# Optimization experiments

Hardware: AMD Instinct MI355X
Metric: run time of the kernel (lower is better)

The kernel has to match this reference:

```python
import jax, jax.numpy as jnp
import numpy as np

B, T, E, H = 2, 2048, 768, 12
DH = E // H  # per-head attention dim
EPS = 1e-5


def setup_inputs() -> dict:
    key = jax.random.key(0)
    ks = jax.random.split(key, 12)
    s = 0.02
    return {
        "x": jax.random.normal(ks[0], (B, T, E), dtype=jnp.float32),
        # stacked per-head projection weights: [H, E, DH], biases [H, DH]
        "Wq": jax.random.normal(ks[1], (H, E, DH), dtype=jnp.float32) * s,
        "bq": jax.random.normal(ks[2], (H, DH), dtype=jnp.float32) * s,
        "Wk": jax.random.normal(ks[3], (H, E, DH), dtype=jnp.float32) * s,
        "bk": jax.random.normal(ks[4], (H, DH), dtype=jnp.float32) * s,
        "Wv": jax.random.normal(ks[5], (H, E, DH), dtype=jnp.float32) * s,
        "bv": jax.random.normal(ks[6], (H, DH), dtype=jnp.float32) * s,
        "Wo": jax.random.normal(ks[7], (E, E), dtype=jnp.float32) * s,
        "bo": jax.random.normal(ks[8], (E,), dtype=jnp.float32) * s,
        "gamma": jnp.ones((E,), dtype=jnp.float32),
        "beta": jnp.zeros((E,), dtype=jnp.float32),
    }


def reference(x, Wq, bq, Wk, bk, Wv, bv, Wo, bo, gamma, beta):
    # per-head projections (heads stacked on axis h)
    q = jnp.einsum("bte,hed->bhtd", x, Wq) + bq[None, :, None, :]
    k = jnp.einsum("bte,hed->bhtd", x, Wk) + bk[None, :, None, :]
    v = jnp.einsum("bte,hed->bhtd", x, Wv) + bv[None, :, None, :]

    scores = jnp.einsum("bhtd,bhsd->bhts", q, k) / jnp.sqrt(jnp.float32(DH))
    causal = jnp.tril(jnp.ones((T, T), dtype=bool))  # True = keep
    scores = jnp.where(causal[None, None], scores, -jnp.inf)
    attn = jax.nn.softmax(scores, axis=-1)
    o = jnp.einsum("bhts,bhsd->bhtd", attn, v)  # [B,H,T,DH]

    # concat heads in head order -> [B,T,E]
    concat = jnp.transpose(o, (0, 2, 1, 3)).reshape(B, T, E)
    proj = concat @ Wo + bo

    # LayerNorm(proj) then residual add
    mu = jnp.mean(proj, axis=-1, keepdims=True)
    var = jnp.mean((proj - mu) ** 2, axis=-1, keepdims=True)
    normed = (proj - mu) * jax.lax.rsqrt(var + EPS) * gamma + beta
    return x + normed
```

## Files before the change

kernel.cpp:

```cpp
#include <hip/hip_runtime.h>
#include <stdint.h>

#define NROWS 4096
#define EMB   768
#define NQKV  2304
#define TSEQ  2048
#define VTSTR 2080
#define XSTR  800
#define WSTR  800
#define PSTR  800
#define NHEAD 12
#define NBH   24

typedef unsigned short u16;
typedef u16  ushort4v __attribute__((ext_vector_type(4)));
typedef u16  ushort8 __attribute__((ext_vector_type(8)));
typedef __bf16 bf16x8 __attribute__((ext_vector_type(8)));
typedef float f32x4 __attribute__((ext_vector_type(4)));

typedef const __attribute__((address_space(1))) void* gas_ptr;
typedef __attribute__((address_space(3))) void* las_ptr;

__device__ __forceinline__ u16 f2bf(float f) {
  union { float f; uint32_t u; } v; v.f = f;
  uint32_t u = v.u;
  return (u16)((u + 0x7fffu + ((u >> 16) & 1u)) >> 16);
}
__device__ __forceinline__ float bf2f(u16 u) {
  union { uint32_t u; float f; } v; v.u = ((uint32_t)u) << 16;
  return v.f;
}
__device__ __forceinline__ uint32_t cvtpk(float lo, float hi) {
  uint32_t r;
  asm("v_cvt_pk_bf16_f32 %0, %1, %2" : "=v"(r) : "v"(lo), "v"(hi));
  return r;
}

#define VMCNT0 asm volatile("s_waitcnt vmcnt(0)" ::: "memory")
#define LGKM0  asm volatile("s_waitcnt lgkmcnt(0)" ::: "memory")
#define SBAR   __builtin_amdgcn_s_barrier()
#define SCHED0 __builtin_amdgcn_sched_barrier(0)
#define MFMA(a, b, c) __builtin_amdgcn_mfma_f32_16x16x32_bf16((a), (b), (c), 0, 0, 0)

__global__ __launch_bounds__(256) void k_pack(const float* __restrict__ x, u16* __restrict__ xb,
                                              const float* __restrict__ Wq, const float* __restrict__ Wk,
                                              const float* __restrict__ Wv, u16* __restrict__ wt,
                                              const float* __restrict__ Wo, u16* __restrict__ wot,
                                              uint32_t* __restrict__ cnt, uint32_t* __restrict__ tbl) {
  int bid = blockIdx.x, tid = threadIdx.x;
  if (bid == 0) {
    if (tid < 8) cnt[tid] = 0;
    if (tid >= 64 && tid < 144) {
      int p = tid - 64;
      int myqb = 0, myc = 0, k = 0;
      for (int qb = 0; qb < 32; ++qb) {
        int nch = (qb + 8) >> 3;
        for (int c = 0; c < nch; ++c) { if (k == p) { myqb = qb; myc = c; } ++k; }
      }
      int t0 = myc * 8;
      int t1 = (myqb + 1 < t0 + 8) ? myqb + 1 : t0 + 8;
      int mylen = t1 - t0, myid = myqb * 4 + myc;
      int rank = 0;
      for (int qb = 0; qb < 32; ++qb) {
        int nch = (qb + 8) >> 3;
        for (int c = 0; c < nch; ++c) {
          int u0 = c * 8;
          int u1 = (qb + 1 < u0 + 8) ? qb + 1 : u0 + 8;
          int l = u1 - u0, id = qb * 4 + c;
          if (l > mylen || (l == mylen && id < myid)) ++rank;
        }
      }
      tbl[rank] = (uint32_t)myqb | ((uint32_t)t0 << 8) | ((uint32_t)t1 << 16)
                | ((uint32_t)myc << 24) | (myqb <= 7 ? 0x80000000u : 0u);
    }
  }
  if (bid < 1536) {
    int i = bid * 2048 + tid * 8;
    int row = i / EMB, col = i - row * EMB;
    float4 a = *(const float4*)(x + i);
    float4 b = *(const float4*)(x + i + 4);
    uint4 o;
    o.x = cvtpk(a.x, a.y); o.y = cvtpk(a.z, a.w);
    o.z = cvtpk(b.x, b.y); o.w = cvtpk(b.z, b.w);
    *(uint4*)(xb + (size_t)row * XSTR + col) = o;
    return;
  }
  __shared__ u16 lds[64][68];
  if (bid < 1968) {
    int t = bid - 1536;
    int sel = t / 144, rest = t - sel * 144;
    int h = rest / 12, ec = rest - h * 12;
    const float* W = sel == 0 ? Wq : (sel == 1 ? Wk : Wv);
    const float* src = W + ((size_t)(h * EMB + ec * 64) * 64);
    int e = tid >> 2, d0 = (tid & 3) * 16;
#pragma unroll
    for (int j = 0; j < 4; ++j) {
      float4 v = *(const float4*)(src + (size_t)e * 64 + d0 + 4 * j);
      ushort4v pk;
      uint32_t w0 = cvtpk(v.x, v.y), w1 = cvtpk(v.z, v.w);
      pk[0] = (u16)(w0 & 0xffff); pk[1] = (u16)(w0 >> 16);
      pk[2] = (u16)(w1 & 0xffff); pk[3] = (u16)(w1 >> 16);
      *(ushort4v*)(&lds[e][d0 + 4 * j]) = pk;
    }
    __syncthreads();
    int d = tid >> 2, e0 = (tid & 3) * 16;
    ushort8 o0, o1;
#pragma unroll
    for (int j = 0; j < 8; ++j) { o0[j] = lds[e0 + j][d]; o1[j] = lds[e0 + 8 + j][d]; }
    int n = sel * EMB + h * 64 + d;
    u16* dst = wt + (size_t)n * WSTR + ec * 64 + e0;
    *(ushort8*)dst = o0;
    *(ushort8*)(dst + 8) = o1;
  } else {
    int t = bid - 1968;
    int er = t / 12, nc = t - er * 12;
    int e = tid >> 2, n0 = (tid & 3) * 16;
#pragma unroll
    for (int j = 0; j < 4; ++j) {
      float4 v = *(const float4*)(Wo + (size_t)(er * 64 + e) * EMB + nc * 64 + n0 + 4 * j);
      ushort4v pk;
      uint32_t w0 = cvtpk(v.x, v.y), w1 = cvtpk(v.z, v.w);
      pk[0] = (u16)(w0 & 0xffff); pk[1] = (u16)(w0 >> 16);
      pk[2] = (u16)(w1 & 0xffff); pk[3] = (u16)(w1 >> 16);
      *(ushort4v*)(&lds[e][n0 + 4 * j]) = pk;
    }
    __syncthreads();
    int n = tid >> 2, e0 = (tid & 3) * 16;
    ushort8 o0, o1;
#pragma unroll
    for (int j = 0; j < 8; ++j) { o0[j] = lds[e0 + j][n]; o1[j] = lds[e0 + 8 + j][n]; }
    u16* dst = wot + (size_t)(nc * 64 + n) * WSTR + er * 64 + e0;
    *(ushort8*)dst = o0;
    *(ushort8*)(dst + 8) = o1;
  }
}

template<int BM, int BN, int OUT_MODE>
__global__ __launch_bounds__(256) void k_gemm(const u16* __restrict__ A, const u16* __restrict__ Bt,
                                              const float* __restrict__ b0, const float* __restrict__ b1,
                                              const float* __restrict__ b2, void* __restrict__ Cout,
                                              u16* __restrict__ qpk, u16* __restrict__ kpk,
                                              u16* __restrict__ vtout,
                                              int M, int N, int K, int lda, int ldb) {
  constexpr int MR = BM / 32, NR = BN / 32;
  __shared__ u16 lds_a[BM * 64];
  __shared__ u16 lds_b[BN * 64];
  int tid = threadIdx.x;
  int w = tid >> 6, lane = tid & 63;
  int wr = w >> 1, wc = w & 1;
  int m0 = blockIdx.x * BM, n0 = blockIdx.y * BN;
  int lrow = lane & 15, g = lane >> 4;

  f32x4 zero = {0.f, 0.f, 0.f, 0.f};
  f32x4 acc[MR][NR];
  for (int m = 0; m < MR; ++m) for (int n = 0; n < NR; ++n) acc[m][n] = zero;

  int l8 = lane >> 3, c8 = lane & 7;

  for (int k0 = 0; k0 < K; k0 += 64) {
#pragma unroll
    for (int i = 0; i < BM / 32; ++i) {
      int row = w * (BM / 4) + 8 * i + l8;
      int c16 = c8 ^ (row & 7);
      const u16* ga = A + (size_t)(m0 + row) * lda + k0 + c16 * 8;
      __builtin_amdgcn_global_load_lds((gas_ptr)ga, (las_ptr)(lds_a + (w * (BM / 4) + 8 * i) * 64), 16, 0, 0);
    }
#pragma unroll
    for (int i = 0; i < BN / 32; ++i) {
      int row = w * (BN / 4) + 8 * i + l8;
      int c16 = c8 ^ (row & 7);
      const u16* gb = Bt + (size_t)(n0 + row) * ldb + k0 + c16 * 8;
      __builtin_amdgcn_global_load_lds((gas_ptr)gb, (las_ptr)(lds_b + (w * (BN / 4) + 8 * i) * 64), 16, 0, 0);
    }
    __syncthreads();
    bf16x8 af[MR][2], bfr[NR][2];
#pragma unroll
    for (int m = 0; m < MR; ++m)
#pragma unroll
      for (int kc = 0; kc < 2; ++kc) {
        int row = wr * (BM / 2) + m * 16 + lrow;
        int ch = (kc * 4 + g) ^ (row & 7);
        af[m][kc] = *(const bf16x8*)(lds_a + row * 64 + ch * 8);
      }
#pragma unroll
    for (int n = 0; n < NR; ++n)
#pragma unroll
      for (int kc = 0; kc < 2; ++kc) {
        int row = wc * (BN / 2) + n * 16 + lrow;
        int ch = (kc * 4 + g) ^ (row & 7);
        bfr[n][kc] = *(const bf16x8*)(lds_b + row * 64 + ch * 8);
      }
#pragma unroll
    for (int kc = 0; kc < 2; ++kc)
#pragma unroll
      for (int m = 0; m < MR; ++m)
#pragma unroll
        for (int n = 0; n < NR; ++n)
          acc[m][n] = MFMA(af[m][kc], bfr[n][kc], acc[m][n]);
    __syncthreads();
  }

#pragma unroll
  for (int m = 0; m < MR; ++m)
#pragma unroll
    for (int n = 0; n < NR; ++n) {
      int col = n0 + wc * (BN / 2) + n * 16 + lrow;
      float bcol;
      if (OUT_MODE == 1) bcol = b0[col];
      else {
        int sel = col >= 1536 ? 2 : (col >= 768 ? 1 : 0);
        const float* bs = sel == 0 ? b0 : (sel == 1 ? b1 : b2);
        bcol = bs[col - sel * EMB];
      }
      int row0 = m0 + wr * (BM / 2) + m * 16 + 4 * g;
      if (OUT_MODE == 2) {
        int sel = col >= 1536 ? 2 : (col >= 768 ? 1 : 0);
        int c = col - sel * EMB;
        int hh = c >> 6, d = c & 63;
        int bb = row0 >> 11, t = row0 & 2047;
        int y = bb * NHEAD + hh;
        if (sel == 2) {
          ushort4v pk;
#pragma unroll
          for (int r = 0; r < 4; ++r) pk[r] = f2bf(acc[m][n][r] + bcol);
          *(ushort4v*)(vtout + (size_t)(y * 64 + d) * VTSTR + t) = pk;
        } else {
          u16* dst = (sel == 0 ? qpk : kpk) + (size_t)(y * TSEQ + t) * 64 + d;
#pragma unroll
          for (int r = 0; r < 4; ++r) dst[r * 64] = f2bf(acc[m][n][r] + bcol);
        }
      } else {
#pragma unroll
        for (int r = 0; r < 4; ++r) {
          int row = row0 + r;
          ((float*)Cout)[(size_t)row * PSTR + col] = acc[m][n][r] + bcol;
        }
      }
    }
}

__global__ __launch_bounds__(256, 4) void k_attn(const u16* __restrict__ qpk, const u16* __restrict__ kpk,
                                                 const u16* __restrict__ vt,
                                                 u16* __restrict__ aout, uint32_t* __restrict__ cnt,
                                                 const uint32_t* __restrict__ tbl,
                                                 u16* __restrict__ pO, float* __restrict__ pL) {
  __shared__ u16 kbuf[2][64 * 64];
  __shared__ u16 vbuf[2][64 * 64];
  __shared__ u16 pbuf[4][16 * 64];
  int tid = threadIdx.x;
  int w = tid >> 6, lane = tid & 63;
  int ql = lane & 15, g = lane >> 4;
  int xcd = blockIdx.x & 7;
  const float sc2 = 0.18033688f;
  u16* pw = &pbuf[w][0];
  int swz = (ql & 7) << 3;
  int l8 = lane >> 3, c8 = lane & 7;
  volatile int* taskp = (volatile int*)&pbuf[0][0];
  f32x4 zero = {0.f, 0.f, 0.f, 0.f};

  for (;;) {
    if (tid == 0) *taskp = (int)atomicAdd(&cnt[xcd], 1u);
    __syncthreads();
    int tau = *taskp;
    __syncthreads();
    if (tau >= 240) break;

    int rank = tau / 3, yl = tau - rank * 3;
    uint32_t te = tbl[rank];
    int qb = te & 0xff, t0 = (te >> 8) & 0xff, t1ex = (te >> 16) & 0xff, cslot = (te >> 24) & 0x7f;
    bool direct = (te >> 31) != 0;

    int y = xcd * 3 + yl;
    int b = y / NHEAD, h = y - b * NHEAD;
    int qrow0w = qb * 64 + w * 16;
    int qg = qrow0w + ql;

    const u16* qp = qpk + (size_t)(y * TSEQ + qg) * 64;
    bf16x8 bq0 = *(const bf16x8*)(qp + g * 8);
    bf16x8 bq1 = *(const bf16x8*)(qp + 32 + g * 8);

    const u16* kst = kpk + (size_t)y * TSEQ * 64;
    const u16* vst = vt + (size_t)y * 64 * VTSTR;

    f32x4 o0 = zero, o1 = zero, o2 = zero, o3 = zero;
    float lr = 0.f;

    auto STAGE = [&](int bi, int t_) {
#pragma unroll
      for (int i = 0; i < 2; ++i) {
        int row = i * 32 + 8 * w + l8;
        int c16 = c8 ^ (row & 7);
        const u16* gk = kst + (size_t)t_ * 4096 + row * 64 + c16 * 8;
        __builtin_amdgcn_global_load_lds((gas_ptr)gk, (las_ptr)(&kbuf[bi][(i * 32 + 8 * w) * 64]), 16, 0, 0);
        const u16* gv = vst + (size_t)row * VTSTR + t_ * 64 + c16 * 8;
        __builtin_amdgcn_global_load_lds((gas_ptr)gv, (las_ptr)(&vbuf[bi][(i * 32 + 8 * w) * 64]), 16, 0, 0);
      }
    };

    STAGE(t0 & 1, t0);
    for (int t = t0; t < t1ex; ++t) {
      int cur = t & 1;
      VMCNT0;
      SBAR;
      if (t + 1 < t1ex) STAGE(cur ^ 1, t + 1);

      const u16* kb = &kbuf[cur][0];
      const u16* vb = &vbuf[cur][0];
      int s0 = t * 64;

      f32x4 st[4];
#pragma unroll
      for (int sblk = 0; sblk < 4; ++sblk) {
        int row = sblk * 16 + ql;
        bf16x8 ka0 = *(const bf16x8*)(kb + ((row * 64 + 8 * g) ^ swz));
        bf16x8 ka1 = *(const bf16x8*)(kb + ((row * 64 + 32 + 8 * g) ^ swz));
        f32x4 acc = zero;
        acc = MFMA(ka0, bq0, acc);
        acc = MFMA(ka1, bq1, acc);
        st[sblk] = acc;
      }

      bool lastt = (t == qb);
      float e[4][4];
#pragma unroll
      for (int sblk = 0; sblk < 4; ++sblk)
#pragma unroll
        for (int r = 0; r < 4; ++r) {
          float vv = __builtin_fmaf(st[sblk][r], sc2, -2.0f);
          if (lastt) {
            int sg = s0 + sblk * 16 + 4 * g + r;
            if (sg > qg) vv = -1e30f;
          }
          float ee = __builtin_amdgcn_exp2f(vv);
          e[sblk][r] = ee;
          lr += ee;
        }

#pragma unroll
      for (int sblk = 0; sblk < 4; ++sblk) {
        uint2 dw;
        dw.x = cvtpk(e[sblk][0], e[sblk][1]);
        dw.y = cvtpk(e[sblk][2], e[sblk][3]);
        *(uint2*)(pw + ((ql * 64 + sblk * 16 + 4 * g) ^ swz)) = dw;
      }
      LGKM0; SCHED0;
      bf16x8 ap0 = *(const bf16x8*)(pw + ((ql * 64 + 8 * g) ^ swz));
      bf16x8 ap1 = *(const bf16x8*)(pw + ((ql * 64 + 32 + 8 * g) ^ swz));

#pragma unroll
      for (int n = 0; n < 4; ++n) {
        int row = n * 16 + ql;
        bf16x8 vb0 = *(const bf16x8*)(vb + ((row * 64 + 8 * g) ^ swz));
        bf16x8 vb1 = *(const bf16x8*)(vb + ((row * 64 + 32 + 8 * g) ^ swz));
        f32x4* op = (n == 0) ? &o0 : (n == 1) ? &o1 : (n == 2) ? &o2 : &o3;
        *op = MFMA(ap0, vb0, *op);
        *op = MFMA(ap1, vb1, *op);
      }
    }

    float lw = lr;
    lw += __shfl_xor(lw, 16);
    lw += __shfl_xor(lw, 32);

    if (direct) {
      float linv = 1.0f / lw;
      float l0 = __shfl(linv, 4 * g + 0);
      float l1 = __shfl(linv, 4 * g + 1);
      float l2 = __shfl(linv, 4 * g + 2);
      float l3 = __shfl(linv, 4 * g + 3);
      u16* ab = aout + (size_t)(b * TSEQ + qrow0w + 4 * g) * XSTR + h * 64 + ql;
      ab[0 * XSTR + 0]  = f2bf(o0[0] * l0); ab[1 * XSTR + 0]  = f2bf(o0[1] * l1);
      ab[2 * XSTR + 0]  = f2bf(o0[2] * l2); ab[3 * XSTR + 0]  = f2bf(o0[3] * l3);
      ab[0 * XSTR + 16] = f2bf(o1[0] * l0); ab[1 * XSTR + 16] = f2bf(o1[1] * l1);
      ab[2 * XSTR + 16] = f2bf(o1[2] * l2); ab[3 * XSTR + 16] = f2bf(o1[3] * l3);
      ab[0 * XSTR + 32] = f2bf(o2[0] * l0); ab[1 * XSTR + 32] = f2bf(o2[1] * l1);
      ab[2 * XSTR + 32] = f2bf(o2[2] * l2); ab[3 * XSTR + 32] = f2bf(o2[3] * l3);
      ab[0 * XSTR + 48] = f2bf(o3[0] * l0); ab[1 * XSTR + 48] = f2bf(o3[1] * l1);
      ab[2 * XSTR + 48] = f2bf(o3[2] * l2); ab[3 * XSTR + 48] = f2bf(o3[3] * l3);
    } else {
      int blk2 = (y * 24 + (qb - 8)) * 4 + cslot;
      u16* po = pO + (size_t)blk2 * 4096;
      float* pl = pL + (size_t)blk2 * 64;
      if (g == 0) pl[w * 16 + ql] = lw;
      u16* pb2 = po + (w * 16 + 4 * g) * 64 + ql;
      pb2[0 * 64 + 0]  = f2bf(o0[0]); pb2[1 * 64 + 0]  = f2bf(o0[1]);
      pb2[2 * 64 + 0]  = f2bf(o0[2]); pb2[3 * 64 + 0]  = f2bf(o0[3]);
      pb2[0 * 64 + 16] = f2bf(o1[0]); pb2[1 * 64 + 16] = f2bf(o1[1]);
      pb2[2 * 64 + 16] = f2bf(o1[2]); pb2[3 * 64 + 16] = f2bf(o1[3]);
      pb2[0 * 64 + 32] = f2bf(o2[0]); pb2[1 * 64 + 32] = f2bf(o2[1]);
      pb2[2 * 64 + 32] = f2bf(o2[2]); pb2[3 * 64 + 32] = f2bf(o2[3]);
      pb2[0 * 64 + 48] = f2bf(o3[0]); pb2[1 * 64 + 48] = f2bf(o3[1]);
      pb2[2 * 64 + 48] = f2bf(o3[2]); pb2[3 * 64 + 48] = f2bf(o3[3]);
    }
  }
}

__global__ __launch_bounds__(256) void k_combine(const u16* __restrict__ pO, const float* __restrict__ pL,
                                                 u16* __restrict__ aout) {
  int blk = blockIdx.x;
  int y = blk / 24, q8 = blk - y * 24, qb = q8 + 8;
  int nch = (qb + 8) >> 3;
  int b = y / NHEAD, h = y - b * NHEAD;
  int tid = threadIdx.x;
  int row = tid >> 2, c0 = (tid & 3) * 16;
  float l = 0.f;
  for (int c = 0; c < nch; ++c) l += pL[((size_t)blk * 4 + c) * 64 + row];
  float rinv = 1.0f / l;
  float acc[16];
#pragma unroll
  for (int j = 0; j < 16; ++j) acc[j] = 0.f;
  for (int c = 0; c < nch; ++c) {
    const u16* p = pO + ((size_t)blk * 4 + c) * 4096 + row * 64 + c0;
    ushort8 a0 = *(const ushort8*)p;
    ushort8 a1 = *(const ushort8*)(p + 8);
#pragma unroll
    for (int j = 0; j < 8; ++j) { acc[j] += bf2f(a0[j]); acc[8 + j] += bf2f(a1[j]); }
  }
  ushort8 o0, o1;
#pragma unroll
  for (int j = 0; j < 8; j += 2) {
    uint32_t w0 = cvtpk(acc[j] * rinv, acc[j + 1] * rinv);
    o0[j] = (u16)(w0 & 0xffff); o0[j + 1] = (u16)(w0 >> 16);
    uint32_t w1 = cvtpk(acc[8 + j] * rinv, acc[9 + j] * rinv);
    o1[j] = (u16)(w1 & 0xffff); o1[j + 1] = (u16)(w1 >> 16);
  }
  u16* dst = aout + (size_t)(b * TSEQ + qb * 64 + row) * XSTR + h * 64 + c0;
  *(ushort8*)dst = o0;
  *(ushort8*)(dst + 8) = o1;
}

__global__ __launch_bounds__(256) void k_ln_res(const float* __restrict__ proj, const float* __restrict__ x,
                                                const float* __restrict__ gamma, const float* __restrict__ beta,
                                                float* __restrict__ out) {
  __shared__ float smem[2][4];
  int row = blockIdx.x;
  const float* pr = proj + (size_t)row * PSTR;
  const float* xr = x + (size_t)row * EMB;
  float* orow = out + (size_t)row * EMB;
  int tid = threadIdx.x;
  float v[3];
  float s = 0.f, s2 = 0.f;
#pragma unroll
  for (int i = 0; i < 3; ++i) { v[i] = pr[tid + 256 * i]; s += v[i]; s2 += v[i] * v[i]; }
#pragma unroll
  for (int m = 1; m < 64; m <<= 1) { s += __shfl_xor(s, m); s2 += __shfl_xor(s2, m); }
  int w = tid >> 6, lane = tid & 63;
  if (lane == 0) { smem[0][w] = s; smem[1][w] = s2; }
  __syncthreads();
  s  = smem[0][0] + smem[0][1] + smem[0][2] + smem[0][3];
  s2 = smem[1][0] + smem[1][1] + smem[1][2] + smem[1][3];
  float mu = s * (1.f / EMB);
  float var = s2 * (1.f / EMB) - mu * mu;
  float rstd = rsqrtf(var + 1e-5f);
#pragma unroll
  for (int i = 0; i < 3; ++i) {
    int c = tid + 256 * i;
    orow[c] = xr[c] + (v[i] - mu) * rstd * gamma[c] + beta[c];
  }
}

extern "C" void kernel_launch(void* const* d_in, const int* in_sizes, int n_in,
                              void* d_out, int out_size, void* d_ws, size_t ws_size,
                              hipStream_t stream) {
  const float* x     = (const float*)d_in[0];
  const float* Wq    = (const float*)d_in[1];
  const float* bq    = (const float*)d_in[2];
  const float* Wk    = (const float*)d_in[3];
  const float* bk    = (const float*)d_in[4];
  const float* Wv    = (const float*)d_in[5];
  const float* bv    = (const float*)d_in[6];
  const float* Wo    = (const float*)d_in[7];
  const float* bo    = (const float*)d_in[8];
  const float* gamma = (const float*)d_in[9];
  const float* beta  = (const float*)d_in[10];
  float* out = (float*)d_out;

  char* ws = (char*)d_ws;
  size_t off = 0;
  u16* xb    = (u16*)(ws + off); off += (size_t)NROWS * XSTR * 2;
  u16* wqkvt = (u16*)(ws + off); off += (size_t)NQKV * WSTR * 2;
  u16* wot   = (u16*)(ws + off); off += (size_t)EMB * WSTR * 2;
  uint32_t* cnt = (uint32_t*)(ws + off); off += 64;
  uint32_t* tbl = (uint32_t*)(ws + off); off += 512;
  u16* qpk   = (u16*)(ws + off); off += (size_t)NBH * TSEQ * 64 * 2;
  u16* kpk   = (u16*)(ws + off); off += (size_t)NBH * TSEQ * 64 * 2;
  u16* vt    = (u16*)(ws + off); off += (size_t)NBH * 64 * VTSTR * 2;
  u16* aout  = (u16*)(ws + off); off += (size_t)NROWS * XSTR * 2;
  u16* pO    = (u16*)(ws + off); off += (size_t)NBH * 24 * 4 * 4096 * 2;
  float* pL  = (float*)(ws + off); off += (size_t)NBH * 24 * 4 * 64 * 4;
  float* proj = (float*)qpk;

  k_pack<<<dim3(2112), 256, 0, stream>>>(x, xb, Wq, Wk, Wv, wqkvt, Wo, wot, cnt, tbl);
  k_gemm<128, 128, 2><<<dim3(NROWS / 128, NQKV / 128), 256, 0, stream>>>(
      xb, wqkvt, bq, bk, bv, nullptr, qpk, kpk, vt, NROWS, NQKV, EMB, XSTR, WSTR);
  k_attn<<<dim3(1024), 256, 0, stream>>>(qpk, kpk, vt, aout, cnt, tbl, pO, pL);
  k_combine<<<dim3(NBH * 24), 256, 0, stream>>>(pO, pL, aout);
  k_gemm<128, 64, 1><<<dim3(NROWS / 128, EMB / 64), 256, 0, stream>>>(
      aout, wot, bo, nullptr, nullptr, proj, nullptr, nullptr, nullptr, NROWS, EMB, EMB, XSTR, WSTR);
  k_ln_res<<<NROWS, 256, 0, stream>>>(proj, x, gamma, beta, out);
}
```

Measured before the change: 130.2 us.

## Enlarge attention query tile to 256 rows with 8 waves, 32 rows each

The attention kernel now processes 256 query rows per task, using 512-thread blocks where each wave handles two 16-row query groups. Each staged K/V tile is therefore reused by four times as many query rows, which cuts global and LDS loads per unit of work. The task table, the split/combine scheme and the workspace layout are rebuilt for the coarser tiles. In exchange there is more wasted masked work on diagonal tiles, fewer and larger tasks (60 per XCD) that may balance worse, and higher register pressure at two blocks per CU.

After: 118.1 us. 1.1x faster.

```diff
diff --git a/kernel.cpp b/kernel.cpp
--- a/kernel.cpp
+++ b/kernel.cpp
@@ -50,28 +50,31 @@
   int bid = blockIdx.x, tid = threadIdx.x;
   if (bid == 0) {
     if (tid < 8) cnt[tid] = 0;
-    if (tid >= 64 && tid < 144) {
+    if (tid >= 64 && tid < 84) {
       int p = tid - 64;
-      int myqb = 0, myc = 0, k = 0;
-      for (int qb = 0; qb < 32; ++qb) {
-        int nch = (qb + 8) >> 3;
-        for (int c = 0; c < nch; ++c) { if (k == p) { myqb = qb; myc = c; } ++k; }
+      int myqi = 0, myc = 0, k = 0;
+      for (int qi = 0; qi < 8; ++qi) {
+        int nt = 4 * qi + 4;
+        int nch = (nt + 7) >> 3;
+        for (int c = 0; c < nch; ++c) { if (k == p) { myqi = qi; myc = c; } ++k; }
       }
+      int nt = 4 * myqi + 4;
       int t0 = myc * 8;
-      int t1 = (myqb + 1 < t0 + 8) ? myqb + 1 : t0 + 8;
-      int mylen = t1 - t0, myid = myqb * 4 + myc;
+      int t1 = (nt < t0 + 8) ? nt : t0 + 8;
+      int mylen = t1 - t0, myid = myqi * 4 + myc;
       int rank = 0;
-      for (int qb = 0; qb < 32; ++qb) {
-        int nch = (qb + 8) >> 3;
+      for (int qi = 0; qi < 8; ++qi) {
+        int nt2 = 4 * qi + 4;
+        int nch = (nt2 + 7) >> 3;
         for (int c = 0; c < nch; ++c) {
           int u0 = c * 8;
-          int u1 = (qb + 1 < u0 + 8) ? qb + 1 : u0 + 8;
-          int l = u1 - u0, id = qb * 4 + c;
+          int u1 = (nt2 < u0 + 8) ? nt2 : u0 + 8;
+          int l = u1 - u0, id = qi * 4 + c;
           if (l > mylen || (l == mylen && id < myid)) ++rank;
         }
       }
-      tbl[rank] = (uint32_t)myqb | ((uint32_t)t0 << 8) | ((uint32_t)t1 << 16)
-                | ((uint32_t)myc << 24) | (myqb <= 7 ? 0x80000000u : 0u);
+      tbl[rank] = (uint32_t)myqi | ((uint32_t)t0 << 8) | ((uint32_t)t1 << 16)
+                | ((uint32_t)myc << 24) | (myqi <= 1 ? 0x80000000u : 0u);
     }
   }
   if (bid < 1536) {
@@ -239,14 +242,55 @@
     }
 }
 
-__global__ __launch_bounds__(256, 4) void k_attn(const u16* __restrict__ qpk, const u16* __restrict__ kpk,
+#define QKROW(SB) do { \
+    bf16x8 ka0 = *(const bf16x8*)(kb + ((((SB) * 16 + ql) * 64 + 8 * g) ^ swz)); \
+    bf16x8 ka1 = *(const bf16x8*)(kb + ((((SB) * 16 + ql) * 64 + 32 + 8 * g) ^ swz)); \
+    st##SB##q0 = MFMA(ka0, bq00, st##SB##q0); st##SB##q0 = MFMA(ka1, bq01, st##SB##q0); \
+    st##SB##q1 = MFMA(ka0, bq10, st##SB##q1); st##SB##q1 = MFMA(ka1, bq11, st##SB##q1); \
+  } while (0)
+
+#define SMX1(STV, SB, QC, LR) do { \
+    float _v0 = __builtin_fmaf(STV[0], sc2, -2.0f); \
+    float _v1 = __builtin_fmaf(STV[1], sc2, -2.0f); \
+    float _v2 = __builtin_fmaf(STV[2], sc2, -2.0f); \
+    float _v3 = __builtin_fmaf(STV[3], sc2, -2.0f); \
+    if (maskt) { \
+      int _sg = s0 + (SB) * 16 + 4 * g; \
+      int _qq = qw0 + (QC) * 16 + ql; \
+      if (_sg + 0 > _qq) _v0 = -1e30f; \
+      if (_sg + 1 > _qq) _v1 = -1e30f; \
+      if (_sg + 2 > _qq) _v2 = -1e30f; \
+      if (_sg + 3 > _qq) _v3 = -1e30f; \
+    } \
+    float _e0 = __builtin_amdgcn_exp2f(_v0), _e1 = __builtin_amdgcn_exp2f(_v1); \
+    float _e2 = __builtin_amdgcn_exp2f(_v2), _e3 = __builtin_amdgcn_exp2f(_v3); \
+    LR += (_e0 + _e1) + (_e2 + _e3); \
+    uint2 _dw; _dw.x = cvtpk(_e0, _e1); _dw.y = cvtpk(_e2, _e3); \
+    *(uint2*)(pw + ((((QC) * 16 + ql) * 64 + (SB) * 16 + 4 * g) ^ swz)) = _dw; \
+  } while (0)
+
+#define PVROW(DB) do { \
+    bf16x8 vb0 = *(const bf16x8*)(vb + ((((DB) * 16 + ql) * 64 + 8 * g) ^ swz)); \
+    bf16x8 vb1 = *(const bf16x8*)(vb + ((((DB) * 16 + ql) * 64 + 32 + 8 * g) ^ swz)); \
+    o##DB##q0 = MFMA(ap00, vb0, o##DB##q0); o##DB##q0 = MFMA(ap01, vb1, o##DB##q0); \
+    o##DB##q1 = MFMA(ap10, vb0, o##DB##q1); o##DB##q1 = MFMA(ap11, vb1, o##DB##q1); \
+  } while (0)
+
+#define OUTD(DB, QC, PTR, STRIDE, L0, L1, L2, L3) do { \
+    (PTR)[0 * (STRIDE) + (DB) * 16] = f2bf(o##DB##q##QC[0] * (L0)); \
+    (PTR)[1 * (STRIDE) + (DB) * 16] = f2bf(o##DB##q##QC[1] * (L1)); \
+    (PTR)[2 * (STRIDE) + (DB) * 16] = f2bf(o##DB##q##QC[2] * (L2)); \
+    (PTR)[3 * (STRIDE) + (DB) * 16] = f2bf(o##DB##q##QC[3] * (L3)); \
+  } while (0)
+
+__global__ __launch_bounds__(512, 2) void k_attn(const u16* __restrict__ qpk, const u16* __restrict__ kpk,
                                                  const u16* __restrict__ vt,
                                                  u16* __restrict__ aout, uint32_t* __restrict__ cnt,
                                                  const uint32_t* __restrict__ tbl,
                                                  u16* __restrict__ pO, float* __restrict__ pL) {
   __shared__ u16 kbuf[2][64 * 64];
   __shared__ u16 vbuf[2][64 * 64];
-  __shared__ u16 pbuf[4][16 * 64];
+  __shared__ u16 pbuf[8][32 * 64];
   int tid = threadIdx.x;
   int w = tid >> 6, lane = tid & 63;
   int ql = lane & 15, g = lane >> 4;
@@ -254,7 +298,7 @@
   const float sc2 = 0.18033688f;
   u16* pw = &pbuf[w][0];
   int swz = (ql & 7) << 3;
-  int l8 = lane >> 3, c8 = lane & 7;
+  int srow = tid >> 3, sc8 = tid & 7;
   volatile int* taskp = (volatile int*)&pbuf[0][0];
   f32x4 zero = {0.f, 0.f, 0.f, 0.f};
 
@@ -263,38 +307,38 @@
     __syncthreads();
     int tau = *taskp;
     __syncthreads();
-    if (tau >= 240) break;
+    if (tau >= 60) break;
 
     int rank = tau / 3, yl = tau - rank * 3;
     uint32_t te = tbl[rank];
-    int qb = te & 0xff, t0 = (te >> 8) & 0xff, t1ex = (te >> 16) & 0xff, cslot = (te >> 24) & 0x7f;
+    int qi = te & 0xff, t0 = (te >> 8) & 0xff, t1ex = (te >> 16) & 0xff, cslot = (te >> 24) & 0x7f;
     bool direct = (te >> 31) != 0;
 
     int y = xcd * 3 + yl;
     int b = y / NHEAD, h = y - b * NHEAD;
-    int qrow0w = qb * 64 + w * 16;
-    int qg = qrow0w + ql;
-
-    const u16* qp = qpk + (size_t)(y * TSEQ + qg) * 64;
-    bf16x8 bq0 = *(const bf16x8*)(qp + g * 8);
-    bf16x8 bq1 = *(const bf16x8*)(qp + 32 + g * 8);
+    int qb0 = qi * 256, qw0 = qb0 + w * 32;
+    int qtw = qw0 >> 6;
+
+    const u16* qp0 = qpk + (size_t)(y * TSEQ + qw0 + ql) * 64;
+    const u16* qp1 = qpk + (size_t)(y * TSEQ + qw0 + 16 + ql) * 64;
+    bf16x8 bq00 = *(const bf16x8*)(qp0 + 8 * g);
+    bf16x8 bq01 = *(const bf16x8*)(qp0 + 32 + 8 * g);
+    bf16x8 bq10 = *(const bf16x8*)(qp1 + 8 * g);
+    bf16x8 bq11 = *(const bf16x8*)(qp1 + 32 + 8 * g);
 
     const u16* kst = kpk + (size_t)y * TSEQ * 64;
     const u16* vst = vt + (size_t)y * 64 * VTSTR;
 
-    f32x4 o0 = zero, o1 = zero, o2 = zero, o3 = zero;
-    float lr = 0.f;
+    f32x4 o0q0 = zero, o1q0 = zero, o2q0 = zero, o3q0 = zero;
+    f32x4 o0q1 = zero, o1q1 = zero, o2q1 = zero, o3q1 = zero;
+    float lr0 = 0.f, lr1 = 0.f;
 
     auto STAGE = [&](int bi, int t_) {
-#pragma unroll
-      for (int i = 0; i < 2; ++i) {
-        int row = i * 32 + 8 * w + l8;
-        int c16 = c8 ^ (row & 7);
-        const u16* gk = kst + (size_t)t_ * 4096 + row * 64 + c16 * 8;
-        __builtin_amdgcn_global_load_lds((gas_ptr)gk, (las_ptr)(&kbuf[bi][(i * 32 + 8 * w) * 64]), 16, 0, 0);
-        const u16* gv = vst + (size_t)row * VTSTR + t_ * 64 + c16 * 8;
-        __builtin_amdgcn_global_load_lds((gas_ptr)gv, (las_ptr)(&vbuf[bi][(i * 32 + 8 * w) * 64]), 16, 0, 0);
-      }
+      int c16 = sc8 ^ (srow & 7);
+      const u16* gk = kst + (size_t)t_ * 4096 + srow * 64 + c16 * 8;
+      __builtin_amdgcn_global_load_lds((gas_ptr)gk, (las_ptr)(&kbuf[bi][(8 * w) * 64]), 16, 0, 0);
+      const u16* gv = vst + (size_t)srow * VTSTR + t_ * 64 + c16 * 8;
+      __builtin_amdgcn_global_load_lds((gas_ptr)gv, (las_ptr)(&vbuf[bi][(8 * w) * 64]), 16, 0, 0);
     };
 
     STAGE(t0 & 1, t0);
@@ -307,90 +351,51 @@
       const u16* kb = &kbuf[cur][0];
       const u16* vb = &vbuf[cur][0];
       int s0 = t * 64;
-
-      f32x4 st[4];
-#pragma unroll
-      for (int sblk = 0; sblk < 4; ++sblk) {
-        int row = sblk * 16 + ql;
-        bf16x8 ka0 = *(const bf16x8*)(kb + ((row * 64 + 8 * g) ^ swz));
-        bf16x8 ka1 = *(const bf16x8*)(kb + ((row * 64 + 32 + 8 * g) ^ swz));
-        f32x4 acc = zero;
-        acc = MFMA(ka0, bq0, acc);
-        acc = MFMA(ka1, bq1, acc);
-        st[sblk] = acc;
-      }
-
-      bool lastt = (t == qb);
-      float e[4][4];
-#pragma unroll
-      for (int sblk = 0; sblk < 4; ++sblk)
-#pragma unroll
-        for (int r = 0; r < 4; ++r) {
-          float vv = __builtin_fmaf(st[sblk][r], sc2, -2.0f);
-          if (lastt) {
-            int sg = s0 + sblk * 16 + 4 * g + r;
-            if (sg > qg) vv = -1e30f;
-          }
-          float ee = __builtin_amdgcn_exp2f(vv);
-          e[sblk][r] = ee;
-          lr += ee;
-        }
-
-#pragma unroll
-      for (int sblk = 0; sblk < 4; ++sblk) {
-        uint2 dw;
-        dw.x = cvtpk(e[sblk][0], e[sblk][1]);
-        dw.y = cvtpk(e[sblk][2], e[sblk][3]);
-        *(uint2*)(pw + ((ql * 64 + sblk * 16 + 4 * g) ^ swz)) = dw;
-      }
+      bool maskt = (t >= qtw);
+
+      f32x4 st0q0 = zero, st1q0 = zero, st2q0 = zero, st3q0 = zero;
+      f32x4 st0q1 = zero, st1q1 = zero, st2q1 = zero, st3q1 = zero;
+      QKROW(0); QKROW(1); QKROW(2); QKROW(3);
+
+      SMX1(st0q0, 0, 0, lr0); SMX1(st1q0, 1, 0, lr0); SMX1(st2q0, 2, 0, lr0); SMX1(st3q0, 3, 0, lr0);
+      SMX1(st0q1, 0, 1, lr1); SMX1(st1q1, 1, 1, lr1); SMX1(st2q1, 2, 1, lr1); SMX1(st3q1, 3, 1, lr1);
+
       LGKM0; SCHED0;
-      bf16x8 ap0 = *(const bf16x8*)(pw + ((ql * 64 + 8 * g) ^ swz));
-      bf16x8 ap1 = *(const bf16x8*)(pw + ((ql * 64 + 32 + 8 * g) ^ swz));
-
-#pragma unroll
-      for (int n = 0; n < 4; ++n) {
-        int row = n * 16 + ql;
-        bf16x8 vb0 = *(const bf16x8*)(vb + ((row * 64 + 8 * g) ^ swz));
-        bf16x8 vb1 = *(const bf16x8*)(vb + ((row * 64 + 32 + 8 * g) ^ swz));
-        f32x4* op = (n == 0) ? &o0 : (n == 1) ? &o1 : (n == 2) ? &o2 : &o3;
-        *op = MFMA(ap0, vb0, *op);
-        *op = MFMA(ap1, vb1, *op);
-      }
-    }
-
-    float lw = lr;
-    lw += __shfl_xor(lw, 16);
-    lw += __shfl_xor(lw, 32);
+      bf16x8 ap00 = *(const bf16x8*)(pw + (((0 * 16 + ql) * 64 + 8 * g) ^ swz));
+      bf16x8 ap01 = *(const bf16x8*)(pw + (((0 * 16 + ql) * 64 + 32 + 8 * g) ^ swz));
+      bf16x8 ap10 = *(const bf16x8*)(pw + (((1 * 16 + ql) * 64 + 8 * g) ^ swz));
+      bf16x8 ap11 = *(const bf16x8*)(pw + (((1 * 16 + ql) * 64 + 32 + 8 * g) ^ swz));
+
+      PVROW(0); PVROW(1); PVROW(2); PVROW(3);
+    }
+
+    float lw0 = lr0, lw1 = lr1;
+    lw0 += __shfl_xor(lw0, 16); lw0 += __shfl_xor(lw0, 32);
+    lw1 += __shfl_xor(lw1, 16); lw1 += __shfl_xor(lw1, 32);
 
     if (direct) {
-      float linv = 1.0f / lw;
-      float l0 = __shfl(linv, 4 * g + 0);
-      float l1 = __shfl(linv, 4 * g + 1);
-      float l2 = __shfl(linv, 4 * g + 2);
-      float l3 = __shfl(linv, 4 * g + 3);
-      u16* ab = aout + (size_t)(b * TSEQ + qrow0w + 4 * g) * XSTR + h * 64 + ql;
-      ab[0 * XSTR + 0]  = f2bf(o0[0] * l0); ab[1 * XSTR + 0]  = f2bf(o0[1] * l1);
-      ab[2 * XSTR + 0]  = f2bf(o0[2] * l2); ab[3 * XSTR + 0]  = f2bf(o0[3] * l3);
-      ab[0 * XSTR + 16] = f2bf(o1[0] * l0); ab[1 * XSTR + 16] = f2bf(o1[1] * l1);
-      ab[2 * XSTR + 16] = f2bf(o1[2] * l2); ab[3 * XSTR + 16] = f2bf(o1[3] * l3);
-      ab[0 * XSTR + 32] = f2bf(o2[0] * l0); ab[1 * XSTR + 32] = f2bf(o2[1] * l1);
-      ab[2 * XSTR + 32] = f2bf(o2[2] * l2); ab[3 * XSTR + 32] = f2bf(o2[3] * l3);
-      ab[0 * XSTR + 48] = f2bf(o3[0] * l0); ab[1 * XSTR + 48] = f2bf(o3[1] * l1);
-      ab[2 * XSTR + 48] = f2bf(o3[2] * l2); ab[3 * XSTR + 48] = f2bf(o3[3] * l3);
+      float li0 = 1.0f / lw0, li1 = 1.0f / lw1;
+      float a0 = __shfl(li0, 4 * g + 0), a1 = __shfl(li0, 4 * g + 1);
+      float a2 = __shfl(li0, 4 * g + 2), a3 = __shfl(li0, 4 * g + 3);
+      u16* ab0 = aout + (size_t)(b * TSEQ + qw0 + 4 * g) * XSTR + h * 64 + ql;
+      OUTD(0, 0, ab0, XSTR, a0, a1, a2, a3); OUTD(1, 0, ab0, XSTR, a0, a1, a2, a3);
+      OUTD(2, 0, ab0, XSTR, a0, a1, a2, a3); OUTD(3, 0, ab0, XSTR, a0, a1, a2, a3);
+      float c0 = __shfl(li1, 4 * g + 0), c1 = __shfl(li1, 4 * g + 1);
+      float c2 = __shfl(li1, 4 * g + 2), c3 = __shfl(li1, 4 * g + 3);
+      u16* ab1 = aout + (size_t)(b * TSEQ + qw0 + 16 + 4 * g) * XSTR + h * 64 + ql;
+      OUTD(0, 1, ab1, XSTR, c0, c1, c2, c3); OUTD(1, 1, ab1, XSTR, c0, c1, c2, c3);
+      OUTD(2, 1, ab1, XSTR, c0, c1, c2, c3); OUTD(3, 1, ab1, XSTR, c0, c1, c2, c3);
     } else {
-      int blk2 = (y * 24 + (qb - 8)) * 4 + cslot;
-      u16* po = pO + (size_t)blk2 * 4096;
-      float* pl = pL + (size_t)blk2 * 64;
-      if (g == 0) pl[w * 16 + ql] = lw;
-      u16* pb2 = po + (w * 16 + 4 * g) * 64 + ql;
-      pb2[0 * 64 + 0]  = f2bf(o0[0]); pb2[1 * 64 + 0]  = f2bf(o0[1]);
-      pb2[2 * 64 + 0]  = f2bf(o0[2]); pb2[3 * 64 + 0]  = f2bf(o0[3]);
-      pb2[0 * 64 + 16] = f2bf(o1[0]); pb2[1 * 64 + 16] = f2bf(o1[1]);
-      pb2[2 * 64 + 16] = f2bf(o1[2]); pb2[3 * 64 + 16] = f2bf(o1[3]);
-      pb2[0 * 64 + 32] = f2bf(o2[0]); pb2[1 * 64 + 32] = f2bf(o2[1]);
-      pb2[2 * 64 + 32] = f2bf(o2[2]); pb2[3 * 64 + 32] = f2bf(o2[3]);
-      pb2[0 * 64 + 48] = f2bf(o3[0]); pb2[1 * 64 + 48] = f2bf(o3[1]);
-      pb2[2 * 64 + 48] = f2bf(o3[2]); pb2[3 * 64 + 48] = f2bf(o3[3]);
+      int blk2 = (y * 8 + qi) * 4 + cslot;
+      u16* po = pO + (size_t)blk2 * 16384;
+      float* pl = pL + (size_t)blk2 * 256;
+      if (g == 0) { pl[w * 32 + ql] = lw0; pl[w * 32 + 16 + ql] = lw1; }
+      u16* pb0 = po + (w * 32 + 4 * g) * 64 + ql;
+      OUTD(0, 0, pb0, 64, 1.f, 1.f, 1.f, 1.f); OUTD(1, 0, pb0, 64, 1.f, 1.f, 1.f, 1.f);
+      OUTD(2, 0, pb0, 64, 1.f, 1.f, 1.f, 1.f); OUTD(3, 0, pb0, 64, 1.f, 1.f, 1.f, 1.f);
+      u16* pb1 = po + (w * 32 + 16 + 4 * g) * 64 + ql;
+      OUTD(0, 1, pb1, 64, 1.f, 1.f, 1.f, 1.f); OUTD(1, 1, pb1, 64, 1.f, 1.f, 1.f, 1.f);
+      OUTD(2, 1, pb1, 64, 1.f, 1.f, 1.f, 1.f); OUTD(3, 1, pb1, 64, 1.f, 1.f, 1.f, 1.f);
     }
   }
 }
@@ -398,24 +403,30 @@
 __global__ __launch_bounds__(256) void k_combine(const u16* __restrict__ pO, const float* __restrict__ pL,
                                                  u16* __restrict__ aout) {
   int blk = blockIdx.x;
-  int y = blk / 24, q8 = blk - y * 24, qb = q8 + 8;
-  int nch = (qb + 8) >> 3;
+  int u = blk >> 2, quarter = blk & 3;
+  int y = u >> 3, qi = u & 7;
+  int nch = (4 * qi + 4 + 7) >> 3;
+  if (nch < 2) return;
   int b = y / NHEAD, h = y - b * NHEAD;
   int tid = threadIdx.x;
-  int row = tid >> 2, c0 = (tid & 3) * 16;
+  int rl = quarter * 64 + (tid >> 2), c0 = (tid & 3) * 16;
   float l = 0.f;
-  for (int c = 0; c < nch; ++c) l += pL[((size_t)blk * 4 + c) * 64 + row];
+#pragma unroll 4
+  for (int c = 0; c < 4; ++c)
+    if (c < nch) l += pL[((size_t)u * 4 + c) * 256 + rl];
   float rinv = 1.0f / l;
   float acc[16];
 #pragma unroll
   for (int j = 0; j < 16; ++j) acc[j] = 0.f;
-  for (int c = 0; c < nch; ++c) {
-    const u16* p = pO + ((size_t)blk * 4 + c) * 4096 + row * 64 + c0;
-    ushort8 a0 = *(const ushort8*)p;
-    ushort8 a1 = *(const ushort8*)(p + 8);
-#pragma unroll
-    for (int j = 0; j < 8; ++j) { acc[j] += bf2f(a0[j]); acc[8 + j] += bf2f(a1[j]); }
-  }
+#pragma unroll 4
+  for (int c = 0; c < 4; ++c)
+    if (c < nch) {
+      const u16* p = pO + ((size_t)u * 4 + c) * 16384 + rl * 64 + c0;
+      ushort8 a0 = *(const ushort8*)p;
+      ushort8 a1 = *(const ushort8*)(p + 8);
+#pragma unroll
+      for (int j = 0; j < 8; ++j) { acc[j] += bf2f(a0[j]); acc[8 + j] += bf2f(a1[j]); }
+    }
   ushort8 o0, o1;
 #pragma unroll
   for (int j = 0; j < 8; j += 2) {
@@ -424,7 +435,7 @@
     uint32_t w1 = cvtpk(acc[8 + j] * rinv, acc[9 + j] * rinv);
     o1[j] = (u16)(w1 & 0xffff); o1[j + 1] = (u16)(w1 >> 16);
   }
-  u16* dst = aout + (size_t)(b * TSEQ + qb * 64 + row) * XSTR + h * 64 + c0;
+  u16* dst = aout + (size_t)(b * TSEQ + qi * 256 + rl) * XSTR + h * 64 + c0;
   *(ushort8*)dst = o0;
   *(ushort8*)(dst + 8) = o1;
 }
@@ -486,15 +497,15 @@
   u16* kpk   = (u16*)(ws + off); off += (size_t)NBH * TSEQ * 64 * 2;
   u16* vt    = (u16*)(ws + off); off += (size_t)NBH * 64 * VTSTR * 2;
   u16* aout  = (u16*)(ws + off); off += (size_t)NROWS * XSTR * 2;
-  u16* pO    = (u16*)(ws + off); off += (size_t)NBH * 24 * 4 * 4096 * 2;
-  float* pL  = (float*)(ws + off); off += (size_t)NBH * 24 * 4 * 64 * 4;
+  u16* pO    = (u16*)(ws + off); off += (size_t)NBH * 8 * 4 * 16384 * 2;
+  float* pL  = (float*)(ws + off); off += (size_t)NBH * 8 * 4 * 256 * 4;
   float* proj = (float*)qpk;
 
   k_pack<<<dim3(2112), 256, 0, stream>>>(x, xb, Wq, Wk, Wv, wqkvt, Wo, wot, cnt, tbl);
   k_gemm<128, 128, 2><<<dim3(NROWS / 128, NQKV / 128), 256, 0, stream>>>(
       xb, wqkvt, bq, bk, bv, nullptr, qpk, kpk, vt, NROWS, NQKV, EMB, XSTR, WSTR);
-  k_attn<<<dim3(1024), 256, 0, stream>>>(qpk, kpk, vt, aout, cnt, tbl, pO, pL);
-  k_combine<<<dim3(NBH * 24), 256, 0, stream>>>(pO, pL, aout);
+  k_attn<<<dim3(512), 512, 0, stream>>>(qpk, kpk, vt, aout, cnt, tbl, pO, pL);
+  k_combine<<<dim3(768), 256, 0, stream>>>(pO, pL, aout);
   k_gemm<128, 64, 1><<<dim3(NROWS / 128, EMB / 64), 256, 0, stream>>>(
       aout, wot, bo, nullptr, nullptr, proj, nullptr, nullptr, nullptr, NROWS, EMB, EMB, XSTR, WSTR);
   k_ln_res<<<NROWS, 256, 0, stream>>>(proj, x, gamma, beta, out);
```
